# Kernel optimization log

Measured on AMD Instinct MI355X. Metric: run time of the kernel, lower is better.

Reference implementation:

```python
import jax, jax.numpy as jnp
import numpy as np

D_MODEL = 1024
NUM_HEADS = 16
D_LATENT = 256
HEAD_DIM = D_MODEL // NUM_HEADS
B, S = 4, 2048


def setup_inputs() -> dict:
    key = jax.random.key(0)
    ks = jax.random.split(key, 11)
    sc_m = 1.0 / np.sqrt(D_MODEL)
    sc_l = 1.0 / np.sqrt(D_LATENT)
    return {
        "x": jax.random.normal(ks[0], (B, S, D_MODEL), dtype=jnp.float32),
        # weights stored as (in, out); equivalent to torch Linear with W^T
        "Wc": jax.random.normal(ks[1], (D_MODEL, D_LATENT), dtype=jnp.float32) * sc_m,
        "bc": jax.random.normal(ks[2], (D_LATENT,), dtype=jnp.float32) * sc_m,
        "Wk": jax.random.normal(ks[3], (D_LATENT, D_MODEL), dtype=jnp.float32) * sc_l,
        "bk": jax.random.normal(ks[4], (D_MODEL,), dtype=jnp.float32) * sc_l,
        "Wv": jax.random.normal(ks[5], (D_LATENT, D_MODEL), dtype=jnp.float32) * sc_l,
        "bv": jax.random.normal(ks[6], (D_MODEL,), dtype=jnp.float32) * sc_l,
        "Wq": jax.random.normal(ks[7], (D_MODEL, D_MODEL), dtype=jnp.float32) * sc_m,
        "bq": jax.random.normal(ks[8], (D_MODEL,), dtype=jnp.float32) * sc_m,
        "Wo": jax.random.normal(ks[9], (D_MODEL, D_MODEL), dtype=jnp.float32) * sc_m,
        "bo": jax.random.normal(ks[10], (D_MODEL,), dtype=jnp.float32) * sc_m,
    }


def reference(x, Wc, bc, Wk, bk, Wv, bv, Wq, bq, Wo, bo):
    b, s, _ = x.shape
    Q = x @ Wq + bq                       # [b,s,d_model]
    kv_latent = x @ Wc + bc               # [b,s,d_latent]
    K = kv_latent @ Wk + bk               # [b,s,d_model]
    V = kv_latent @ Wv + bv               # [b,s,d_model]
    # split heads -> [b,h,s,hd]
    Q = Q.reshape(b, s, NUM_HEADS, HEAD_DIM).transpose(0, 2, 1, 3)
    K = K.reshape(b, s, NUM_HEADS, HEAD_DIM).transpose(0, 2, 1, 3)
    V = V.reshape(b, s, NUM_HEADS, HEAD_DIM).transpose(0, 2, 1, 3)
    scores = jnp.einsum("bhqd,bhkd->bhqk", Q, K) / np.sqrt(HEAD_DIM)
    attn = jax.nn.softmax(scores, axis=-1)  # dropout p=0.0 (eval) -> identity
    out = jnp.einsum("bhqk,bhkd->bhqd", attn, V)
    out = out.transpose(0, 2, 1, 3).reshape(b, s, D_MODEL)
    return out @ Wo + bo
```

## Files before the change

kernel.cpp:

```cpp
#include <hip/hip_runtime.h>

typedef __bf16 bf16;
typedef __bf16 bf16x4 __attribute__((ext_vector_type(4)));
typedef __bf16 bf16x8 __attribute__((ext_vector_type(8)));
typedef float f32x4 __attribute__((ext_vector_type(4)));

#define NHEADS 16
#define HDIM 64
#define SEQ 2048
#define BATCH 4
#define DMODEL 1024
#define NTOK (BATCH * SEQ)
#define KVBLK 64
#define QSCALE 0.18033688f
#define C0EXP  -28.853901f

typedef void gvoid __attribute__((address_space(1)));
typedef void lvoid __attribute__((address_space(3)));

__device__ __forceinline__ f32x4 mfma16(bf16x8 a, bf16x8 b, f32x4 c) {
  return __builtin_amdgcn_mfma_f32_16x16x32_bf16(a, b, c, 0, 0, 0);
}

__device__ __forceinline__ void gload16(const bf16* g, bf16* l) {
  __builtin_amdgcn_global_load_lds((gvoid*)g, (lvoid*)l, 16, 0, 0);
}

__device__ __forceinline__ void tr32(const float* in, bf16* out, int K, int N,
                                     int bx, int by, int tid) {
  __shared__ float t[32][33];
  const int x = tid & 31, y = tid >> 5;
  const int n0 = bx * 32, k0 = by * 32;
  for (int i = y; i < 32; i += 8)
    t[i][x] = in[(long)(k0 + i) * N + n0 + x];
  __syncthreads();
  for (int i = y; i < 32; i += 8)
    out[(long)(n0 + i) * K + k0 + x] = (bf16)t[x][i];
}

__global__ __launch_bounds__(256) void prep_all(
    const float* __restrict__ x,  const float* __restrict__ Wc,
    const float* __restrict__ Wk, const float* __restrict__ Wv,
    const float* __restrict__ Wq, const float* __restrict__ Wo,
    bf16* __restrict__ xb, bf16* __restrict__ WqcT,
    bf16* __restrict__ WkvT, bf16* __restrict__ WoT) {
  const int b = blockIdx.x;
  const int tid = threadIdx.x;
  if (b < 1024) {
    tr32(Wq, WqcT, 1024, 1024, b & 31, b >> 5, tid);
  } else if (b < 1280) {
    const int bb = b - 1024;
    tr32(Wc, WqcT + 1024 * 1024, 1024, 256, bb & 7, bb >> 3, tid);
  } else if (b < 1536) {
    const int bb = b - 1280;
    tr32(Wk, WkvT, 256, 1024, bb & 31, bb >> 5, tid);
  } else if (b < 1792) {
    const int bb = b - 1536;
    tr32(Wv, WkvT + 1024 * 256, 256, 1024, bb & 31, bb >> 5, tid);
  } else if (b < 2816) {
    const int bb = b - 1792;
    tr32(Wo, WoT, 1024, 1024, bb & 31, bb >> 5, tid);
  } else {
    const long i = ((long)(b - 2816) * 256 + tid) * 8;
    const float4 a = *(const float4*)(x + i);
    const float4 c = *(const float4*)(x + i + 4);
    bf16x8 o;
    o[0] = (bf16)a.x; o[1] = (bf16)a.y; o[2] = (bf16)a.z; o[3] = (bf16)a.w;
    o[4] = (bf16)c.x; o[5] = (bf16)c.y; o[6] = (bf16)c.z; o[7] = (bf16)c.w;
    *(bf16x8*)(xb + i) = o;
  }
}

template <int MODE, typename OutT>
__global__ __launch_bounds__(256) void gemm_bt(
    const bf16* __restrict__ A, const bf16* __restrict__ Bt,
    const float* __restrict__ bias, const float* __restrict__ bias2,
    OutT* __restrict__ D, bf16* __restrict__ D2, int N, int K) {
  __shared__ bf16 smem[3 * 4096 * 2];
  bf16* const AsB = smem;
  bf16* const BsB = smem + 3 * 4096;
  const int tid = threadIdx.x;
  const int lane = tid & 63;
  const int wave = tid >> 6;
  const int wr = (wave >> 1) * 64;
  const int wc = (wave & 1) * 64;
  const int r16 = lane & 15;
  const int kg = lane >> 4;
  const long rowBase = (long)blockIdx.x * 128;
  const long colBase = (long)blockIdx.y * 128;

  const int o0 = tid * 16;
  const int o1 = o0 + 4096;
  const int ra0 = o0 >> 6, ra1 = o1 >> 6;
  const int ca0 = ((o0 & 63) ^ (((ra0 >> 1) & 3) << 4)) >> 1;
  const int ca1 = ((o1 & 63) ^ (((ra1 >> 1) & 3) << 4)) >> 1;
  const bf16* pA0 = A + (rowBase + ra0) * K + ca0;
  const bf16* pA1 = A + (rowBase + ra1) * K + ca1;
  const bf16* pB0 = Bt + (colBase + ra0) * K + ca0;
  const bf16* pB1 = Bt + (colBase + ra1) * K + ca1;
  const int e0 = o0 >> 1, e1 = o1 >> 1;

  auto gaddr = [](const bf16* base, int row, int bytecol) -> const bf16* {
    return base + row * 32 + ((bytecol ^ (((row >> 1) & 3) << 4)) >> 1);
  };

  f32x4 acc[4][4] = {};
  const int nk = K >> 5;

#define GSTAGE(kt_)                                        \
  {                                                        \
    const int b_ = (kt_) % 3;                              \
    const int o_ = (kt_) * 32;                             \
    gload16(pA0 + o_, AsB + b_ * 4096 + e0);               \
    gload16(pA1 + o_, AsB + b_ * 4096 + e1);               \
    gload16(pB0 + o_, BsB + b_ * 4096 + e0);               \
    gload16(pB1 + o_, BsB + b_ * 4096 + e1);               \
  }

  GSTAGE(0);
  GSTAGE(1);
  asm volatile("s_waitcnt vmcnt(4)" ::: "memory");
  asm volatile("s_barrier" ::: "memory");

  for (int kt = 0; kt < nk; ++kt) {
    if (kt + 2 < nk) {
      GSTAGE(kt + 2);
      asm volatile("s_waitcnt vmcnt(4)" ::: "memory");
    } else {
      asm volatile("s_waitcnt vmcnt(0)" ::: "memory");
    }
    const bf16* as = AsB + (kt % 3) * 4096;
    const bf16* bs = BsB + (kt % 3) * 4096;
    bf16x8 af[4], bfr[4];
#pragma unroll
    for (int m = 0; m < 4; ++m)
      af[m] = *(const bf16x8*)gaddr(as, wr + m * 16 + r16, kg * 16);
#pragma unroll
    for (int n = 0; n < 4; ++n)
      bfr[n] = *(const bf16x8*)gaddr(bs, wc + n * 16 + r16, kg * 16);
    __builtin_amdgcn_s_setprio(1);
#pragma unroll
    for (int m = 0; m < 4; ++m)
#pragma unroll
      for (int n = 0; n < 4; ++n)
        acc[m][n] = mfma16(af[m], bfr[n], acc[m][n]);
    __builtin_amdgcn_s_setprio(0);
    asm volatile("s_barrier" ::: "memory");
  }
#undef GSTAGE

  if (MODE == 0) {
#pragma unroll
    for (int n = 0; n < 4; ++n) {
      const long col = colBase + wc + n * 16 + r16;
      const float bvv = bias[col];
#pragma unroll
      for (int m = 0; m < 4; ++m) {
        const long row0 = rowBase + wr + m * 16 + kg * 4;
#pragma unroll
        for (int r = 0; r < 4; ++r)
          D[(row0 + r) * N + col] = (OutT)(acc[m][n][r] + bvv);
      }
    }
  } else {
    const bool tr = (MODE == 4) && (colBase >= 1024);
    bf16* E = smem;
#pragma unroll
    for (int n = 0; n < 4; ++n) {
      const int cl = wc + n * 16 + r16;
      const long col = colBase + cl;
      const bool primary = col < 1024;
      const float bvv = primary ? bias[col] : bias2[col - 1024];
#pragma unroll
      for (int m = 0; m < 4; ++m) {
#pragma unroll
        for (int r = 0; r < 4; ++r) {
          const int rl = wr + m * 16 + kg * 4 + r;
          float v = acc[m][n][r] + bvv;
          if (MODE == 3 && primary) v *= QSCALE;
          if (tr) E[cl * 136 + rl] = (bf16)v;
          else    E[rl * 136 + cl] = (bf16)v;
        }
      }
    }
    __syncthreads();
    const int er = tid >> 1;
    const int c0 = (tid & 1) * 64;
    const long brow = rowBase >> 11;
    const int srow = (int)(rowBase & 2047);
    bf16* dp;
    if (!tr) {
      if (colBase < 1024) {
        const long col = colBase + c0;
        dp = (bf16*)(void*)D +
             (((brow * NHEADS + (col >> 6)) * SEQ) + srow + er) * HDIM;
      } else {
        dp = D2 + (long)(rowBase + er) * 256 + (colBase - 1024) + c0;
      }
    } else {
      const long c2 = colBase - 1024 + er;
      dp = D2 + ((brow * NHEADS + (c2 >> 6)) * HDIM + (c2 & 63)) * SEQ +
           srow + c0;
    }
    const bf16* Er = E + er * 136 + c0;
#pragma unroll
    for (int j = 0; j < 8; ++j)
      *(bf16x8*)(dp + j * 8) = *(const bf16x8*)(Er + j * 8);
  }
}

__global__ __launch_bounds__(512, 4) void mla_attn(
    const bf16* __restrict__ Q, const bf16* __restrict__ Kg,
    const bf16* __restrict__ Vt, bf16* __restrict__ Out) {
  __shared__ bf16 Kl[3][KVBLK * HDIM];
  __shared__ bf16 Vl[3][HDIM * KVBLK];
  __shared__ bf16 Pl[8][32][64];
  const int tid = threadIdx.x;
  const int lane = tid & 63;
  const int w = tid >> 6;
  const int r16 = lane & 15;
  const int kg = lane >> 4;
  const int bid = (int)blockIdx.x;
  const int lb = (bid & 7) * 64 + (bid >> 3);
  const int qb = lb & 7;
  const int bh = lb >> 3;
  const bf16* Qp = Q + (long)bh * SEQ * HDIM;
  const bf16* Kp = Kg + (long)bh * SEQ * HDIM;
  const bf16* Vp = Vt + (long)bh * HDIM * SEQ;
  const int q0 = qb * 256 + w * 32;

  const int so = tid * 16;
  const int srow = so >> 7;
  const int scol = ((so & 127) ^ ((srow & 7) << 4)) >> 1;
  const bf16* KgS = Kp + (long)srow * HDIM + scol;
  const bf16* VgS = Vp + (long)srow * SEQ + scol;
  const int se = so >> 1;

  bf16x8 aq[2][2];
#pragma unroll
  for (int qm = 0; qm < 2; ++qm) {
    const bf16* qp = Qp + (long)(q0 + qm * 16 + r16) * HDIM + kg * 8;
    aq[qm][0] = *(const bf16x8*)qp;
    aq[qm][1] = *(const bf16x8*)(qp + 32);
  }

  bf16x8 kones;
#pragma unroll
  for (int j = 0; j < 8; ++j) kones[j] = (bf16)1.0f;

  f32x4 accO[2][4];
  f32x4 lsumv[2] = {{0.f, 0.f, 0.f, 0.f}, {0.f, 0.f, 0.f, 0.f}};
#pragma unroll
  for (int qm = 0; qm < 2; ++qm)
#pragma unroll
    for (int dt = 0; dt < 4; ++dt) accO[qm][dt] = (f32x4){0.f, 0.f, 0.f, 0.f};
  const f32x4 c0v = {C0EXP, C0EXP, C0EXP, C0EXP};

  auto kaddr = [](const bf16* base, int row, int bytecol) -> const bf16* {
    return base + row * 64 + ((bytecol ^ ((row & 7) << 4)) >> 1);
  };

#define ASTAGE(t_)                                                   \
  {                                                                  \
    const int b_ = (t_) % 3;                                         \
    const long off_ = (long)(t_) * KVBLK;                            \
    gload16(KgS + off_ * HDIM, (bf16*)Kl[b_] + se);                  \
    gload16(VgS + off_, (bf16*)Vl[b_] + se);                         \
  }

  ASTAGE(0);
  ASTAGE(1);
  asm volatile("s_waitcnt vmcnt(2)" ::: "memory");
  asm volatile("s_barrier" ::: "memory");

  const int NT = SEQ / KVBLK;
  for (int t = 0; t < NT; ++t) {
    if (t + 2 < NT) {
      ASTAGE(t + 2);
      asm volatile("s_waitcnt vmcnt(2)" ::: "memory");
    } else {
      asm volatile("s_waitcnt vmcnt(0)" ::: "memory");
    }
    const bf16* kl = Kl[t % 3];
    const bf16* vl = Vl[t % 3];
    f32x4 sc[2][4];
    __builtin_amdgcn_s_setprio(1);
#pragma unroll
    for (int kt = 0; kt < 4; ++kt) {
      const int row = kt * 16 + r16;
      const bf16x8 kf0 = *(const bf16x8*)kaddr(kl, row, kg * 16);
      const bf16x8 kf1 = *(const bf16x8*)kaddr(kl, row, 64 + kg * 16);
#pragma unroll
      for (int qm = 0; qm < 2; ++qm) {
        f32x4 tv = mfma16(kf0, aq[qm][0], c0v);
        tv = mfma16(kf1, aq[qm][1], tv);
        sc[qm][kt] = tv;
      }
    }
    __builtin_amdgcn_s_setprio(0);
#pragma unroll
    for (int qm = 0; qm < 2; ++qm) {
      bf16* prow = &Pl[w][qm * 16 + r16][0];
      const int sw = (r16 & 7) << 4;
#pragma unroll
      for (int kt = 0; kt < 4; ++kt) {
        bf16x4 pk;
#pragma unroll
        for (int r = 0; r < 4; ++r)
          pk[r] = (bf16)__builtin_amdgcn_exp2f(sc[qm][kt][r]);
        *(bf16x4*)((char*)prow + ((kt * 32 + kg * 8) ^ sw)) = pk;
      }
    }
    __builtin_amdgcn_s_setprio(1);
#pragma unroll
    for (int kc = 0; kc < 2; ++kc) {
      bf16x8 ap[2];
#pragma unroll
      for (int qm = 0; qm < 2; ++qm) {
        const bf16* prow = &Pl[w][qm * 16 + r16][0];
        const int sw = (r16 & 7) << 4;
        ap[qm] = *(const bf16x8*)((const char*)prow + ((kc * 64 + kg * 16) ^ sw));
      }
      lsumv[0] = mfma16(ap[0], kones, lsumv[0]);
      lsumv[1] = mfma16(ap[1], kones, lsumv[1]);
#pragma unroll
      for (int dt = 0; dt < 4; ++dt) {
        const int vrow = dt * 16 + r16;
        const bf16x8 vf = *(const bf16x8*)kaddr(vl, vrow, kc * 64 + kg * 16);
        accO[0][dt] = mfma16(ap[0], vf, accO[0][dt]);
        accO[1][dt] = mfma16(ap[1], vf, accO[1][dt]);
      }
    }
    __builtin_amdgcn_s_setprio(0);
    asm volatile("s_barrier" ::: "memory");
  }
#undef ASTAGE

  const int b = bh >> 4, h = bh & 15;
#pragma unroll
  for (int qm = 0; qm < 2; ++qm)
#pragma unroll
    for (int r = 0; r < 4; ++r) {
      const float inv = 1.f / lsumv[qm][r];
      const long qrow = q0 + qm * 16 + kg * 4 + r;
      bf16* op = Out + ((long)b * SEQ + qrow) * DMODEL + h * HDIM;
#pragma unroll
      for (int dt = 0; dt < 4; ++dt)
        op[dt * 16 + r16] = (bf16)(accO[qm][dt][r] * inv);
    }
}

extern "C" void kernel_launch(void* const* d_in, const int* in_sizes, int n_in,
                              void* d_out, int out_size, void* d_ws, size_t ws_size,
                              hipStream_t stream) {
  const float* x  = (const float*)d_in[0];
  const float* Wc = (const float*)d_in[1];
  const float* bc = (const float*)d_in[2];
  const float* Wk = (const float*)d_in[3];
  const float* bk = (const float*)d_in[4];
  const float* Wv = (const float*)d_in[5];
  const float* bv = (const float*)d_in[6];
  const float* Wq = (const float*)d_in[7];
  const float* bq = (const float*)d_in[8];
  const float* Wo = (const float*)d_in[9];
  const float* bo = (const float*)d_in[10];
  float* out = (float*)d_out;

  bf16* p = (bf16*)d_ws;
  bf16* xb   = p; p += (long)NTOK * 1024;
  bf16* WqcT = p; p += 1280 * 1024;
  bf16* WkvT = p; p += 2048 * 256;
  bf16* WoT  = p; p += 1024 * 1024;
  bf16* Qb   = p; p += (long)NTOK * 1024;
  bf16* Kb   = p; p += (long)NTOK * 1024;
  bf16* Vtb  = p; p += (long)NTOK * 1024;
  bf16* Cb   = p; p += (long)NTOK * 256;
  bf16* AO   = xb;

  prep_all<<<6912, 256, 0, stream>>>(x, Wc, Wk, Wv, Wq, Wo, xb, WqcT, WkvT, WoT);

  gemm_bt<3, bf16><<<dim3(64, 10), 256, 0, stream>>>(xb, WqcT, bq, bc, Qb, Cb, 1280, 1024);
  gemm_bt<4, bf16><<<dim3(64, 16), 256, 0, stream>>>(Cb, WkvT, bk, bv, Kb, Vtb, 2048, 256);

  mla_attn<<<(SEQ / 256) * BATCH * NHEADS, 512, 0, stream>>>(Qb, Kb, Vtb, AO);

  gemm_bt<0, float><<<dim3(64, 8), 256, 0, stream>>>(AO, WoT, bo, bo, out, (bf16*)nullptr, 1024, 1024);
}
```

Before: 171.7 us.

## Switch attention to 32x32 MFMA and keep probabilities in registers via permlane swap

The attention kernel now uses 32x32x16 bf16 MFMA instructions in place of 16x16x32, with each wave computing a 32-query tile against K sub-blocks of 32 rows. The exponentiated scores are packed to bf16 with v_cvt_pk_bf16_f32 and rearranged across lane halves with v_permlane32_swap, so they can feed the PV MFMA directly. This removes the per-wave LDS P buffer and its write/read round trip. The cost is larger accumulator register footprint, which may affect occupancy under the 512x4 launch bounds, and the code relies on the exact register layout of the 32x32 MFMA.

```diff
diff --git a/kernel.cpp b/kernel.cpp
--- a/kernel.cpp
+++ b/kernel.cpp
@@ -4,6 +4,7 @@
 typedef __bf16 bf16x4 __attribute__((ext_vector_type(4)));
 typedef __bf16 bf16x8 __attribute__((ext_vector_type(8)));
 typedef float f32x4 __attribute__((ext_vector_type(4)));
+typedef float f32x16 __attribute__((ext_vector_type(16)));
 
 #define NHEADS 16
 #define HDIM 64
@@ -22,8 +23,21 @@
   return __builtin_amdgcn_mfma_f32_16x16x32_bf16(a, b, c, 0, 0, 0);
 }
 
+__device__ __forceinline__ f32x16 mfma32(bf16x8 a, bf16x8 b, f32x16 c) {
+  return __builtin_amdgcn_mfma_f32_32x32x16_bf16(a, b, c, 0, 0, 0);
+}
+
 __device__ __forceinline__ void gload16(const bf16* g, bf16* l) {
   __builtin_amdgcn_global_load_lds((gvoid*)g, (lvoid*)l, 16, 0, 0);
+}
+
+__device__ __forceinline__ unsigned cvtpk(float a, float b) {
+  unsigned r;
+  asm("v_cvt_pk_bf16_f32 %0, %1, %2" : "=v"(r) : "v"(a), "v"(b));
+  return r;
+}
+__device__ __forceinline__ void swap32(unsigned& a, unsigned& b) {
+  asm("v_permlane32_swap_b32 %0, %1" : "+v"(a), "+v"(b));
 }
 
 __device__ __forceinline__ void tr32(const float* in, bf16* out, int K, int N,
@@ -214,12 +228,11 @@
     const bf16* __restrict__ Vt, bf16* __restrict__ Out) {
   __shared__ bf16 Kl[3][KVBLK * HDIM];
   __shared__ bf16 Vl[3][HDIM * KVBLK];
-  __shared__ bf16 Pl[8][32][64];
   const int tid = threadIdx.x;
   const int lane = tid & 63;
   const int w = tid >> 6;
-  const int r16 = lane & 15;
-  const int kg = lane >> 4;
+  const int l31 = lane & 31;
+  const int hi = lane >> 5;
   const int bid = (int)blockIdx.x;
   const int lb = (bid & 7) * 64 + (bid >> 3);
   const int qb = lb & 7;
@@ -236,25 +249,21 @@
   const bf16* VgS = Vp + (long)srow * SEQ + scol;
   const int se = so >> 1;
 
-  bf16x8 aq[2][2];
-#pragma unroll
-  for (int qm = 0; qm < 2; ++qm) {
-    const bf16* qp = Qp + (long)(q0 + qm * 16 + r16) * HDIM + kg * 8;
-    aq[qm][0] = *(const bf16x8*)qp;
-    aq[qm][1] = *(const bf16x8*)(qp + 32);
-  }
+  bf16x8 aq[4];
+#pragma unroll
+  for (int ks = 0; ks < 4; ++ks)
+    aq[ks] = *(const bf16x8*)(Qp + (long)(q0 + l31) * HDIM + ks * 16 + hi * 8);
 
   bf16x8 kones;
 #pragma unroll
   for (int j = 0; j < 8; ++j) kones[j] = (bf16)1.0f;
 
-  f32x4 accO[2][4];
-  f32x4 lsumv[2] = {{0.f, 0.f, 0.f, 0.f}, {0.f, 0.f, 0.f, 0.f}};
-#pragma unroll
-  for (int qm = 0; qm < 2; ++qm)
-#pragma unroll
-    for (int dt = 0; dt < 4; ++dt) accO[qm][dt] = (f32x4){0.f, 0.f, 0.f, 0.f};
-  const f32x4 c0v = {C0EXP, C0EXP, C0EXP, C0EXP};
+  f32x16 accO[2], lsum;
+#pragma unroll
+  for (int i = 0; i < 16; ++i) { accO[0][i] = 0.f; accO[1][i] = 0.f; lsum[i] = 0.f; }
+  f32x16 c0v;
+#pragma unroll
+  for (int i = 0; i < 16; ++i) c0v[i] = C0EXP;
 
   auto kaddr = [](const bf16* base, int row, int bytecol) -> const bf16* {
     return base + row * 64 + ((bytecol ^ ((row & 7) << 4)) >> 1);
@@ -283,52 +292,45 @@
     }
     const bf16* kl = Kl[t % 3];
     const bf16* vl = Vl[t % 3];
-    f32x4 sc[2][4];
+
+    unsigned pk[2][8];
+#pragma unroll
+    for (int kb = 0; kb < 2; ++kb) {
+      f32x16 sc = c0v;
+      __builtin_amdgcn_s_setprio(1);
+#pragma unroll
+      for (int ks = 0; ks < 4; ++ks) {
+        const bf16x8 kf = *(const bf16x8*)kaddr(kl, kb * 32 + l31, ks * 32 + hi * 16);
+        sc = mfma32(kf, aq[ks], sc);
+      }
+      __builtin_amdgcn_s_setprio(0);
+#pragma unroll
+      for (int i = 0; i < 8; ++i)
+        pk[kb][i] = cvtpk(__builtin_amdgcn_exp2f(sc[2 * i]),
+                          __builtin_amdgcn_exp2f(sc[2 * i + 1]));
+      swap32(pk[kb][0], pk[kb][2]);
+      swap32(pk[kb][1], pk[kb][3]);
+      swap32(pk[kb][4], pk[kb][6]);
+      swap32(pk[kb][5], pk[kb][7]);
+    }
+
     __builtin_amdgcn_s_setprio(1);
 #pragma unroll
-    for (int kt = 0; kt < 4; ++kt) {
-      const int row = kt * 16 + r16;
-      const bf16x8 kf0 = *(const bf16x8*)kaddr(kl, row, kg * 16);
-      const bf16x8 kf1 = *(const bf16x8*)kaddr(kl, row, 64 + kg * 16);
-#pragma unroll
-      for (int qm = 0; qm < 2; ++qm) {
-        f32x4 tv = mfma16(kf0, aq[qm][0], c0v);
-        tv = mfma16(kf1, aq[qm][1], tv);
-        sc[qm][kt] = tv;
-      }
-    }
-    __builtin_amdgcn_s_setprio(0);
-#pragma unroll
-    for (int qm = 0; qm < 2; ++qm) {
-      bf16* prow = &Pl[w][qm * 16 + r16][0];
-      const int sw = (r16 & 7) << 4;
-#pragma unroll
-      for (int kt = 0; kt < 4; ++kt) {
-        bf16x4 pk;
-#pragma unroll
-        for (int r = 0; r < 4; ++r)
-          pk[r] = (bf16)__builtin_amdgcn_exp2f(sc[qm][kt][r]);
-        *(bf16x4*)((char*)prow + ((kt * 32 + kg * 8) ^ sw)) = pk;
-      }
-    }
-    __builtin_amdgcn_s_setprio(1);
-#pragma unroll
-    for (int kc = 0; kc < 2; ++kc) {
-      bf16x8 ap[2];
-#pragma unroll
-      for (int qm = 0; qm < 2; ++qm) {
-        const bf16* prow = &Pl[w][qm * 16 + r16][0];
-        const int sw = (r16 & 7) << 4;
-        ap[qm] = *(const bf16x8*)((const char*)prow + ((kc * 64 + kg * 16) ^ sw));
-      }
-      lsumv[0] = mfma16(ap[0], kones, lsumv[0]);
-      lsumv[1] = mfma16(ap[1], kones, lsumv[1]);
-#pragma unroll
-      for (int dt = 0; dt < 4; ++dt) {
-        const int vrow = dt * 16 + r16;
-        const bf16x8 vf = *(const bf16x8*)kaddr(vl, vrow, kc * 64 + kg * 16);
-        accO[0][dt] = mfma16(ap[0], vf, accO[0][dt]);
-        accO[1][dt] = mfma16(ap[1], vf, accO[1][dt]);
+    for (int kb = 0; kb < 2; ++kb) {
+#pragma unroll
+      for (int ks2 = 0; ks2 < 2; ++ks2) {
+        union { unsigned u[4]; bf16x8 v; } ap;
+        ap.u[0] = pk[kb][ks2 * 4 + 0];
+        ap.u[1] = pk[kb][ks2 * 4 + 1];
+        ap.u[2] = pk[kb][ks2 * 4 + 2];
+        ap.u[3] = pk[kb][ks2 * 4 + 3];
+        lsum = mfma32(ap.v, kones, lsum);
+#pragma unroll
+        for (int dt = 0; dt < 2; ++dt) {
+          const bf16x8 vf = *(const bf16x8*)kaddr(
+              vl, dt * 32 + l31, kb * 64 + ks2 * 32 + hi * 16);
+          accO[dt] = mfma32(ap.v, vf, accO[dt]);
+        }
       }
     }
     __builtin_amdgcn_s_setprio(0);
@@ -338,16 +340,14 @@
 
   const int b = bh >> 4, h = bh & 15;
 #pragma unroll
-  for (int qm = 0; qm < 2; ++qm)
-#pragma unroll
-    for (int r = 0; r < 4; ++r) {
-      const float inv = 1.f / lsumv[qm][r];
-      const long qrow = q0 + qm * 16 + kg * 4 + r;
-      bf16* op = Out + ((long)b * SEQ + qrow) * DMODEL + h * HDIM;
-#pragma unroll
-      for (int dt = 0; dt < 4; ++dt)
-        op[dt * 16 + r16] = (bf16)(accO[qm][dt][r] * inv);
-    }
+  for (int r = 0; r < 16; ++r) {
+    const float inv = 1.f / lsum[r];
+    const int q = (r & 3) + 8 * (r >> 2) + 4 * hi;
+    bf16* op = Out + ((long)b * SEQ + q0 + q) * DMODEL + h * HDIM;
+#pragma unroll
+    for (int dt = 0; dt < 2; ++dt)
+      op[dt * 32 + l31] = (bf16)(accO[dt][r] * inv);
+  }
 }
 
 extern "C" void kernel_launch(void* const* d_in, const int* in_sizes, int n_in,
```

After: 219.8 us. +28.0%, slower.
